# Kernel optimization log

Hardware: AMD Instinct MI355X
Metric: run time of the kernel (lower is better)

Reference implementation:

```python
import jax, jax.numpy as jnp
from jax import lax
import numpy as np

B, N, NPOINT, NSAMPLE = 16, 4096, 1024, 32
RADIUS = 0.2
D_FEAT = 64
IN_CH = 3 + D_FEAT
MLP = (64, 64, 128)
EPS = 1e-5


def fps(xyz, npoint):
    # farthest point sampling, xyz: [B,N,3] -> idx [B,npoint] (start at index 0)
    Bn, Nn, _ = xyz.shape
    batch = jnp.arange(Bn)

    def step(carry, _):
        dist, far = carry                      # dist [B,N], far [B]
        centroid = xyz[batch, far]             # [B,3]
        d = jnp.sum((xyz - centroid[:, None, :]) ** 2, -1)
        dist = jnp.minimum(dist, d)
        new_far = jnp.argmax(dist, -1).astype(jnp.int32)
        return (dist, new_far), far

    init = (jnp.full((Bn, Nn), 1e10, xyz.dtype), jnp.zeros((Bn,), jnp.int32))
    _, idxs = lax.scan(step, init, None, length=npoint)
    return jnp.transpose(idxs)                 # [B, npoint]


def square_distance(a, b):
    # a [B,S,3], b [B,N,3] -> [B,S,N]
    return (jnp.sum(a * a, -1)[:, :, None]
            + jnp.sum(b * b, -1)[:, None, :]
            - 2.0 * jnp.einsum('bsc,bnc->bsn', a, b))


def query_ball(radius, nsample, xyz, new_xyz):
    Nn = xyz.shape[1]
    sqr = square_distance(new_xyz, xyz)                      # [B,S,N]
    gi = jnp.where(sqr > radius ** 2, Nn, jnp.arange(Nn, dtype=jnp.int32))
    gi = jnp.sort(gi, axis=-1)[:, :, :nsample]               # [B,S,K]
    first = gi[:, :, :1]
    return jnp.where(gi == Nn, first, gi)


def gather_points(pts, idx):
    # pts [B,N,C], idx [B,...] -> [B,...,C]
    return jax.vmap(lambda p, i: p[i])(pts, idx)


def _forward(xyz, points, params):
    x = jnp.transpose(xyz, (0, 2, 1))          # [B,N,3]
    p = jnp.transpose(points, (0, 2, 1))       # [B,N,D]
    fidx = fps(x, NPOINT)                      # [B,S]
    new_xyz = gather_points(x, fidx)           # [B,S,3]
    idx = query_ball(RADIUS, NSAMPLE, x, new_xyz)  # [B,S,K]
    g_xyz = gather_points(x, idx)              # [B,S,K,3]
    g_norm = g_xyz - new_xyz[:, :, None, :]
    g_pts = gather_points(p, idx)              # [B,S,K,D]
    feat = jnp.concatenate([g_norm, g_pts], -1)  # [B,S,K,3+D]
    h = jnp.transpose(feat, (0, 3, 2, 1))      # [B,C,K,S]
    for (w, b, g, bt) in params:
        h = jnp.einsum('bcks,oc->boks', h, w) + b[None, :, None, None]
        m = jnp.mean(h, axis=(0, 2, 3), keepdims=True)
        v = jnp.mean((h - m) ** 2, axis=(0, 2, 3), keepdims=True)  # biased var (train BN)
        h = g[None, :, None, None] * (h - m) * lax.rsqrt(v + EPS) + bt[None, :, None, None]
        h = jax.nn.relu(h)
    new_points = jnp.max(h, axis=2)            # [B,Cout,S]
    return jnp.transpose(new_xyz, (0, 2, 1)), new_points


def setup_inputs() -> dict:
    key = jax.random.key(0)
    ks = jax.random.split(key, 16)
    xyz = jax.random.uniform(ks[0], (B, 3, N), dtype=jnp.float32)
    points = jax.random.normal(ks[1], (B, D_FEAT, N), dtype=jnp.float32)
    inp = {'xyz': xyz, 'points': points}
    cin = IN_CH
    for l, cout in enumerate(MLP):
        scale = 1.0 / np.sqrt(cin)
        inp[f'w{l}'] = jax.random.normal(ks[2 + 4 * l], (cout, cin), dtype=jnp.float32) * scale
        inp[f'b{l}'] = jax.random.normal(ks[3 + 4 * l], (cout,), dtype=jnp.float32) * scale
        inp[f'g{l}'] = jnp.ones((cout,), jnp.float32)
        inp[f'bt{l}'] = jnp.zeros((cout,), jnp.float32)
        cin = cout
    return inp


def reference(xyz, points, w0, b0, g0, bt0, w1, b1, g1, bt1, w2, b2, g2, bt2):
    params = [(w0, b0, g0, bt0), (w1, b1, g1, bt1), (w2, b2, g2, bt2)]
    return _forward(xyz, points, params)
```

## Files before the change

kernel.cpp:

```cpp
#include <hip/hip_runtime.h>
#include <stdint.h>

#define NB    16
#define NN    4096
#define NP    1024
#define NS    32
#define NGRP  (NB*NP)
#define CNT   524288.0

typedef short  bf16x8 __attribute__((ext_vector_type(8)));
typedef float  f32x4  __attribute__((ext_vector_type(4)));

__device__ __forceinline__ float bf2f(unsigned short u) {
    return __uint_as_float(((unsigned)u) << 16);
}
__device__ __forceinline__ unsigned short f2bf(float f) {
    unsigned u = __float_as_uint(f);
    unsigned r = u + 0x7fffu + ((u >> 16) & 1u);
    return (unsigned short)(r >> 16);
}
__device__ __forceinline__ bf16x8 as_bf(uint4 u) {
    union { uint4 a; bf16x8 b; } c; c.a = u; return c.b;
}

template <int CTRL, int RM>
__device__ __forceinline__ unsigned long long dppmax(unsigned long long k) {
    int lo = (int)(unsigned)k;
    int hi = (int)(k >> 32);
    int ml = __builtin_amdgcn_update_dpp(lo, lo, CTRL, RM, 0xf, false);
    int mh = __builtin_amdgcn_update_dpp(hi, hi, CTRL, RM, 0xf, false);
    unsigned long long m = ((unsigned long long)(unsigned)mh << 32) | (unsigned)ml;
    return m > k ? m : k;
}

__global__ __launch_bounds__(256, 1) void fps_t_kernel(const float* __restrict__ xyz,
                                                       const float* __restrict__ points,
                                                       const float* __restrict__ w0,
                                                       int* __restrict__ fidx,
                                                       unsigned short* __restrict__ T) {
    if (blockIdx.x >= 16) {
        int gid = (blockIdx.x - 16) * 256 + threadIdx.x;
        int b = gid >> 12, n = gid & (NN - 1);
        const float* xb = xyz + (size_t)b * 3 * NN;
        const float* pb = points + (size_t)b * 64 * NN;
        float acc[64];
#pragma unroll
        for (int o = 0; o < 64; o++) acc[o] = 0.f;
        for (int c = 0; c < 67; c++) {
            float v = (c < 3) ? xb[c * NN + n] : pb[(c - 3) * NN + n];
#pragma unroll
            for (int o = 0; o < 64; o++) acc[o] = fmaf(v, w0[o * 67 + c], acc[o]);
        }
        unsigned short* dst = T + (size_t)gid * 64;
        for (int oo = 0; oo < 64; oo += 8) {
            union { unsigned short u[8]; uint4 v; } r;
#pragma unroll
            for (int j = 0; j < 8; j++) r.u[j] = f2bf(acc[oo + j]);
            *(uint4*)&dst[oo] = r.v;
        }
        return;
    }
    int b = blockIdx.x, tid = threadIdx.x;
    const float* xb = xyz + (size_t)b * 3 * NN;
    __shared__ float4 sxyz4[NN];
    __shared__ unsigned long long red[2][4];
    __shared__ int fbuf[NP];
    float px[16], py[16], pz[16], dist[16];
#pragma unroll
    for (int i = 0; i < 16; i++) {
        int n = i * 256 + tid;
        px[i] = xb[n]; py[i] = xb[NN + n]; pz[i] = xb[2 * NN + n];
        sxyz4[n] = make_float4(px[i], py[i], pz[i], 0.f);
        dist[i] = 1e10f;
    }
#pragma unroll
    for (int i = 0; i < 16; i++) {
        asm volatile("" : "+v"(px[i]));
        asm volatile("" : "+v"(py[i]));
        asm volatile("" : "+v"(pz[i]));
    }
    int wv = tid >> 6;
    if (tid == 0) fbuf[0] = 0;
    int far = 0;
    __syncthreads();
    for (int t = 0; t < NP; t++) {
        float4 c = sxyz4[far];
        float cx = c.x, cy = c.y, cz = c.z;
        float bv = -1.0f; int bi = 0;
#pragma unroll
        for (int i = 0; i < 16; i++) {
            float dx = __fsub_rn(px[i], cx);
            float dy = __fsub_rn(py[i], cy);
            float dz = __fsub_rn(pz[i], cz);
            float d = __fadd_rn(__fadd_rn(__fmul_rn(dx, dx), __fmul_rn(dy, dy)),
                                __fmul_rn(dz, dz));
            float nd = fminf(dist[i], d);
            dist[i] = nd;
            if (nd > bv) { bv = nd; bi = i; }
        }
        int n_best = bi * 256 + tid;
        unsigned long long k =
            ((unsigned long long)__float_as_uint(bv) << 32) |
            (unsigned long long)(~(unsigned)n_best);
        k = dppmax<0x111, 0xf>(k);
        k = dppmax<0x112, 0xf>(k);
        k = dppmax<0x114, 0xf>(k);
        k = dppmax<0x118, 0xf>(k);
        k = dppmax<0x142, 0xa>(k);
        k = dppmax<0x143, 0xc>(k);
        if ((tid & 63) == 63) red[t & 1][wv] = k;
        __syncthreads();
        ulonglong2 ra = *(ulonglong2*)&red[t & 1][0];
        ulonglong2 rb = *(ulonglong2*)&red[t & 1][2];
        unsigned long long r0 = ra.x, r1 = ra.y, r2 = rb.x, r3 = rb.y;
        if (r1 > r0) r0 = r1;
        if (r3 > r2) r2 = r3;
        if (r2 > r0) r0 = r2;
        far = (int)(~(unsigned)r0);
        if (tid == 0 && t + 1 < NP) fbuf[t + 1] = far;
    }
    __syncthreads();
    for (int i = tid; i < NP; i += 256) fidx[b * NP + i] = fbuf[i];
}

__global__ __launch_bounds__(256) void group_kernel(const float* __restrict__ xyz,
                                                    const unsigned short* __restrict__ T,
                                                    const int* __restrict__ fidx,
                                                    int* __restrict__ idx,
                                                    const float* __restrict__ w0,
                                                    const float* __restrict__ b0,
                                                    double* __restrict__ stage1,
                                                    float* __restrict__ out0) {
    __shared__ int gidx[4][NS];
    int t = threadIdx.x, wv = t >> 6, lane = t & 63;
    int g = blockIdx.x * 4 + wv;
    int b = g >> 10, s = g & 1023;
    const float* xb = xyz + (size_t)b * 3 * NN;
    int fid = fidx[g];
    float cx = xb[fid], cy = xb[NN + fid], cz = xb[2 * NN + fid];
    if (lane < 3) {
        float v = (lane == 0) ? cx : ((lane == 1) ? cy : cz);
        out0[((size_t)b * 3 + lane) * NP + s] = v;
    }
    float sa = __fadd_rn(__fadd_rn(__fmul_rn(cx, cx), __fmul_rn(cy, cy)),
                         __fmul_rn(cz, cz));
    int* out = idx + (size_t)g * NS;
    int total = 0; int first = 0;
    for (int ci = 0; ci < NN / 64; ci++) {
        int n = ci * 64 + lane;
        float x = xb[n], y = xb[NN + n], z = xb[2 * NN + n];
        float sb = __fadd_rn(__fadd_rn(__fmul_rn(x, x), __fmul_rn(y, y)),
                             __fmul_rn(z, z));
        float dot = __fadd_rn(__fadd_rn(__fmul_rn(x, cx), __fmul_rn(y, cy)),
                              __fmul_rn(z, cz));
        float sqr = __fsub_rn(__fadd_rn(sa, sb), __fmul_rn(2.0f, dot));
        bool pred = !(sqr > 0.04f);
        unsigned long long mask = __ballot(pred);
        if (mask) {
            if (total == 0) first = ci * 64 + (int)__builtin_ctzll(mask);
            int pos = total + (int)__popcll(mask & ((1ull << lane) - 1ull));
            if (pred && pos < NS) { out[pos] = n; gidx[wv][pos] = n; }
            total += (int)__popcll(mask);
            if (total >= NS) break;
        }
    }
    if (total < NS) {
        if (lane >= total && lane < NS) { out[lane] = first; gidx[wv][lane] = first; }
    }
    int o = lane;
    float uo = fmaf(w0[o * 67 + 2], cz, fmaf(w0[o * 67 + 1], cy, w0[o * 67] * cx));
    float bo = b0[o];
    const unsigned short* Tb = T + (size_t)b * NN * 64;
    float s1 = 0.f, s2 = 0.f;
    for (int k = 0; k < NS; k++) {
        int n = gidx[wv][k];
        float tv = bf2f(Tb[(size_t)n * 64 + o]);
        float h = tv - uo + bo;
        s1 += h; s2 = fmaf(h, h, s2);
    }
    int slot = g & 63;
    atomicAdd(&stage1[slot * 128 + o], (double)s1);
    atomicAdd(&stage1[slot * 128 + 64 + o], (double)s2);
}

__global__ void finalize_kernel(const double* __restrict__ stage, int C,
                                const float* __restrict__ gamma,
                                const float* __restrict__ beta,
                                float* __restrict__ AB) {
    int o = threadIdx.x;
    double s = 0.0, q = 0.0;
    for (int i = 0; i < 64; i++) {
        s += stage[i * 2 * C + o];
        q += stage[i * 2 * C + C + o];
    }
    double m = s * (1.0 / CNT);
    double v = q * (1.0 / CNT) - m * m;
    double A = (double)gamma[o] / sqrt(v + 1e-5);
    AB[o] = (float)A;
    AB[C + o] = (float)((double)beta[o] - m * A);
}

__global__ __launch_bounds__(256) void layer2_kernel(const float* __restrict__ xyz,
                                                     const unsigned short* __restrict__ T,
                                                     const int* __restrict__ fidx,
                                                     const int* __restrict__ idx,
                                                     const float* __restrict__ w0,
                                                     const float* __restrict__ b0,
                                                     const float* __restrict__ AB1,
                                                     const float* __restrict__ w1,
                                                     const float* __restrict__ b1,
                                                     unsigned short* __restrict__ h2,
                                                     double* __restrict__ stage2) {
    __shared__ __attribute__((aligned(16))) unsigned short w1s[64][72];
    __shared__ __attribute__((aligned(16))) unsigned short h1s[4][32][72];
    __shared__ float psum[64], psq[64];
    int t = threadIdx.x, wv = t >> 6, lane = t & 63;
    int quad = lane >> 4, col = lane & 15;
    int g = blockIdx.x * 4 + wv;
    int b = g >> 10;
    for (int lin = t; lin < 4096; lin += 256)
        w1s[lin >> 6][lin & 63] = f2bf(w1[lin]);
    if (t < 64) { psum[t] = 0.f; psq[t] = 0.f; }
    {
        int fid = fidx[g];
        const float* xb = xyz + (size_t)b * 3 * NN;
        float cx = xb[fid], cy = xb[NN + fid], cz = xb[2 * NN + fid];
        int o = lane;
        float uo = fmaf(w0[o * 67 + 2], cz, fmaf(w0[o * 67 + 1], cy, w0[o * 67] * cx));
        float bo = b0[o];
        float a1 = AB1[o], bb1 = AB1[64 + o];
        const int* gi = idx + (size_t)g * NS;
        const unsigned short* Tb = T + (size_t)b * NN * 64;
        for (int k = 0; k < NS; k++) {
            int n = gi[k];
            float tv = bf2f(Tb[(size_t)n * 64 + o]);
            float h = tv - uo + bo;
            float hn = fmaxf(fmaf(h, a1, bb1), 0.f);
            h1s[wv][k][o] = f2bf(hn);
        }
    }
    __syncthreads();
    f32x4 acc[2][4];
#pragma unroll
    for (int i = 0; i < 2; i++)
#pragma unroll
        for (int j = 0; j < 4; j++) acc[i][j] = (f32x4){0.f, 0.f, 0.f, 0.f};
#pragma unroll
    for (int ks = 0; ks < 2; ks++) {
        bf16x8 a0 = as_bf(*(const uint4*)&h1s[wv][col][ks * 32 + quad * 8]);
        bf16x8 a1f = as_bf(*(const uint4*)&h1s[wv][16 + col][ks * 32 + quad * 8]);
#pragma unroll
        for (int nt = 0; nt < 4; nt++) {
            bf16x8 bf = as_bf(*(const uint4*)&w1s[nt * 16 + col][ks * 32 + quad * 8]);
            acc[0][nt] = __builtin_amdgcn_mfma_f32_16x16x32_bf16(a0, bf, acc[0][nt], 0, 0, 0);
            acc[1][nt] = __builtin_amdgcn_mfma_f32_16x16x32_bf16(a1f, bf, acc[1][nt], 0, 0, 0);
        }
    }
    float s1[4], s2[4];
#pragma unroll
    for (int nt = 0; nt < 4; nt++) {
        float bb = b1[nt * 16 + col];
        s1[nt] = 0.f; s2[nt] = 0.f;
#pragma unroll
        for (int mt = 0; mt < 2; mt++)
#pragma unroll
            for (int r = 0; r < 4; r++) {
                float v = acc[mt][nt][r] + bb;
                s1[nt] += v; s2[nt] = fmaf(v, v, s2[nt]);
                h1s[wv][mt * 16 + quad * 4 + r][nt * 16 + col] = f2bf(v);
            }
        s1[nt] += __shfl_xor(s1[nt], 16); s1[nt] += __shfl_xor(s1[nt], 32);
        s2[nt] += __shfl_xor(s2[nt], 16); s2[nt] += __shfl_xor(s2[nt], 32);
        if (quad == 0) {
            atomicAdd(&psum[nt * 16 + col], s1[nt]);
            atomicAdd(&psq[nt * 16 + col], s2[nt]);
        }
    }
#pragma unroll
    for (int r = 0; r < 4; r++) {
        int lin = lane + 64 * r;
        int row = lin >> 3, c = lin & 7;
        uint4 v = *(const uint4*)&h1s[wv][row][c * 8];
        *(uint4*)&h2[((size_t)g * NS + row) * 64 + c * 8] = v;
    }
    __syncthreads();
    if (t < 64) {
        int slot = blockIdx.x & 63;
        atomicAdd(&stage2[slot * 128 + t], (double)psum[t]);
        atomicAdd(&stage2[slot * 128 + 64 + t], (double)psq[t]);
    }
}

__global__ __launch_bounds__(256) void layer3_kernel(const unsigned short* __restrict__ h2,
                                                     const float* __restrict__ AB2,
                                                     const float* __restrict__ w2,
                                                     const float* __restrict__ b2,
                                                     double* __restrict__ stage3,
                                                     float* __restrict__ mxbuf,
                                                     float* __restrict__ mnbuf) {
    __shared__ __attribute__((aligned(16))) unsigned short w2s[128][72];
    __shared__ __attribute__((aligned(16))) unsigned short h2s[4][32][72];
    __shared__ float psum[128], psq[128];
    int t = threadIdx.x, wv = t >> 6, lane = t & 63;
    int quad = lane >> 4, col = lane & 15;
    int g = blockIdx.x * 4 + wv;
    for (int lin = t; lin < 8192; lin += 256)
        w2s[lin >> 6][lin & 63] = f2bf(w2[lin]);
    if (t < 128) { psum[t] = 0.f; psq[t] = 0.f; }
    {
        int c = lane & 7;
        float a2v[8], bb2v[8];
#pragma unroll
        for (int j = 0; j < 8; j++) {
            a2v[j] = AB2[c * 8 + j];
            bb2v[j] = AB2[64 + c * 8 + j];
        }
        const unsigned short* hg = h2 + (size_t)g * NS * 64;
#pragma unroll
        for (int r = 0; r < 4; r++) {
            int row = (lane >> 3) + 8 * r;
            union { uint4 v; unsigned short u[8]; } in, outp;
            in.v = *(const uint4*)&hg[row * 64 + c * 8];
#pragma unroll
            for (int j = 0; j < 8; j++) {
                float f = bf2f(in.u[j]);
                outp.u[j] = f2bf(fmaxf(fmaf(f, a2v[j], bb2v[j]), 0.f));
            }
            *(uint4*)&h2s[wv][row][c * 8] = outp.v;
        }
    }
    __syncthreads();
    f32x4 acc[2][8];
#pragma unroll
    for (int i = 0; i < 2; i++)
#pragma unroll
        for (int j = 0; j < 8; j++) acc[i][j] = (f32x4){0.f, 0.f, 0.f, 0.f};
#pragma unroll
    for (int ks = 0; ks < 2; ks++) {
        bf16x8 a0 = as_bf(*(const uint4*)&h2s[wv][col][ks * 32 + quad * 8]);
        bf16x8 a1f = as_bf(*(const uint4*)&h2s[wv][16 + col][ks * 32 + quad * 8]);
#pragma unroll
        for (int nt = 0; nt < 8; nt++) {
            bf16x8 bf = as_bf(*(const uint4*)&w2s[nt * 16 + col][ks * 32 + quad * 8]);
            acc[0][nt] = __builtin_amdgcn_mfma_f32_16x16x32_bf16(a0, bf, acc[0][nt], 0, 0, 0);
            acc[1][nt] = __builtin_amdgcn_mfma_f32_16x16x32_bf16(a1f, bf, acc[1][nt], 0, 0, 0);
        }
    }
#pragma unroll
    for (int nt = 0; nt < 8; nt++) {
        float bb = b2[nt * 16 + col];
        float s1 = 0.f, s2 = 0.f, mx = -1e30f, mn = 1e30f;
#pragma unroll
        for (int mt = 0; mt < 2; mt++)
#pragma unroll
            for (int r = 0; r < 4; r++) {
                float v = acc[mt][nt][r] + bb;
                s1 += v; s2 = fmaf(v, v, s2);
                mx = fmaxf(mx, v); mn = fminf(mn, v);
            }
        s1 += __shfl_xor(s1, 16); s1 += __shfl_xor(s1, 32);
        s2 += __shfl_xor(s2, 16); s2 += __shfl_xor(s2, 32);
        mx = fmaxf(mx, __shfl_xor(mx, 16)); mx = fmaxf(mx, __shfl_xor(mx, 32));
        mn = fminf(mn, __shfl_xor(mn, 16)); mn = fminf(mn, __shfl_xor(mn, 32));
        if (quad == 0) {
            atomicAdd(&psum[nt * 16 + col], s1);
            atomicAdd(&psq[nt * 16 + col], s2);
            mxbuf[(size_t)g * 128 + nt * 16 + col] = mx;
            mnbuf[(size_t)g * 128 + nt * 16 + col] = mn;
        }
    }
    __syncthreads();
    if (t < 128) {
        int slot = blockIdx.x & 63;
        atomicAdd(&stage3[slot * 256 + t], (double)psum[t]);
        atomicAdd(&stage3[slot * 256 + 128 + t], (double)psq[t]);
    }
}

__global__ __launch_bounds__(256) void epilogue_kernel(const float* __restrict__ mxbuf,
                                                       const float* __restrict__ mnbuf,
                                                       const float* __restrict__ AB3,
                                                       float* __restrict__ out1) {
    __shared__ float tile[32][65];
    int blk = blockIdx.x;
    int b = blk >> 6; int rem = blk & 63;
    int o0 = (rem >> 4) * 32; int s0 = (rem & 15) * 64;
    int t = threadIdx.x;
#pragma unroll
    for (int j = 0; j < 8; j++) {
        int lin = t + 256 * j;
        int sl = lin >> 5, ol = lin & 31;
        int o = o0 + ol;
        float a = AB3[o], bb = AB3[128 + o];
        size_t src = ((size_t)b * NP + s0 + sl) * 128 + o;
        float v = (a >= 0.f) ? mxbuf[src] : mnbuf[src];
        tile[ol][sl] = fmaxf(fmaf(v, a, bb), 0.f);
    }
    __syncthreads();
#pragma unroll
    for (int j = 0; j < 8; j++) {
        int lin = t + 256 * j;
        int ol = lin >> 6, sl = lin & 63;
        out1[((size_t)b * 128 + o0 + ol) * NP + s0 + sl] = tile[ol][sl];
    }
}

extern "C" void kernel_launch(void* const* d_in, const int* in_sizes, int n_in,
                              void* d_out, int out_size, void* d_ws, size_t ws_size,
                              hipStream_t stream) {
    const float* xyz    = (const float*)d_in[0];
    const float* points = (const float*)d_in[1];
    const float* w0  = (const float*)d_in[2];
    const float* b0  = (const float*)d_in[3];
    const float* g0  = (const float*)d_in[4];
    const float* bt0 = (const float*)d_in[5];
    const float* w1  = (const float*)d_in[6];
    const float* b1  = (const float*)d_in[7];
    const float* g1  = (const float*)d_in[8];
    const float* bt1 = (const float*)d_in[9];
    const float* w2  = (const float*)d_in[10];
    const float* b2  = (const float*)d_in[11];
    const float* g2  = (const float*)d_in[12];
    const float* bt2 = (const float*)d_in[13];

    char* ws = (char*)d_ws;
    int*            fidx = (int*)(ws + 0);
    int*            idx  = (int*)(ws + 65536);
    unsigned short* T    = (unsigned short*)(ws + 2162688);
    unsigned short* h2   = (unsigned short*)(ws + 10551296);
    float*          mxbuf = (float*)(ws + 77660160);
    float*          mnbuf = (float*)(ws + 86048768);
    double*         stage = (double*)(ws + 94437376);
    float*          AB   = (float*)(ws + 94699520);
    double* stage1 = stage;
    double* stage2 = stage + 64 * 128;
    double* stage3 = stage + 2 * 64 * 128;
    float* AB1 = AB; float* AB2 = AB + 128; float* AB3 = AB + 256;
    float* out0 = (float*)d_out;
    float* out1 = out0 + NB * 3 * NP;

    hipMemsetAsync(stage, 0, 262144, stream);

    fps_t_kernel<<<16 + 256, 256, 0, stream>>>(xyz, points, w0, fidx, T);
    group_kernel<<<NGRP / 4, 256, 0, stream>>>(xyz, T, fidx, idx, w0, b0, stage1, out0);
    finalize_kernel<<<1, 64, 0, stream>>>(stage1, 64, g0, bt0, AB1);
    layer2_kernel<<<NGRP / 4, 256, 0, stream>>>(xyz, T, fidx, idx, w0, b0, AB1,
                                                w1, b1, h2, stage2);
    finalize_kernel<<<1, 64, 0, stream>>>(stage2, 64, g1, bt1, AB2);
    layer3_kernel<<<NGRP / 4, 256, 0, stream>>>(h2, AB2, w2, b2, stage3, mxbuf, mnbuf);
    finalize_kernel<<<1, 128, 0, stream>>>(stage3, 128, g2, bt2, AB3);
    epilogue_kernel<<<1024, 256, 0, stream>>>(mxbuf, mnbuf, AB3, out1);
}
```

Measured before the change: 836.0 us.

## Fuse FPS, first-layer transform and grouping into one persistent kernel with flag-based streaming

```diff
diff --git a/kernel.cpp b/kernel.cpp
--- a/kernel.cpp
+++ b/kernel.cpp
@@ -7,6 +7,7 @@
 #define NS    32
 #define NGRP  (NB*NP)
 #define CNT   524288.0
+#define NWRK  240
 
 typedef short  bf16x8 __attribute__((ext_vector_type(8)));
 typedef float  f32x4  __attribute__((ext_vector_type(4)));
@@ -33,154 +34,177 @@
     return m > k ? m : k;
 }
 
-__global__ __launch_bounds__(256, 1) void fps_t_kernel(const float* __restrict__ xyz,
+__global__ __launch_bounds__(256, 1) void fused_kernel(const float* __restrict__ xyz,
                                                        const float* __restrict__ points,
                                                        const float* __restrict__ w0,
+                                                       const float* __restrict__ b0,
                                                        int* __restrict__ fidx,
-                                                       unsigned short* __restrict__ T) {
-    if (blockIdx.x >= 16) {
-        int gid = (blockIdx.x - 16) * 256 + threadIdx.x;
-        int b = gid >> 12, n = gid & (NN - 1);
-        const float* xb = xyz + (size_t)b * 3 * NN;
-        const float* pb = points + (size_t)b * 64 * NN;
-        float acc[64];
-#pragma unroll
-        for (int o = 0; o < 64; o++) acc[o] = 0.f;
-        for (int c = 0; c < 67; c++) {
-            float v = (c < 3) ? xb[c * NN + n] : pb[(c - 3) * NN + n];
-#pragma unroll
-            for (int o = 0; o < 64; o++) acc[o] = fmaf(v, w0[o * 67 + c], acc[o]);
-        }
-        unsigned short* dst = T + (size_t)gid * 64;
-        for (int oo = 0; oo < 64; oo += 8) {
-            union { unsigned short u[8]; uint4 v; } r;
-#pragma unroll
-            for (int j = 0; j < 8; j++) r.u[j] = f2bf(acc[oo + j]);
-            *(uint4*)&dst[oo] = r.v;
-        }
-        return;
-    }
-    int b = blockIdx.x, tid = threadIdx.x;
-    const float* xb = xyz + (size_t)b * 3 * NN;
+                                                       unsigned short* __restrict__ T,
+                                                       int* __restrict__ idx,
+                                                       double* __restrict__ stage1,
+                                                       float* __restrict__ out0,
+                                                       int* __restrict__ sync_ctr) {
     __shared__ float4 sxyz4[NN];
     __shared__ unsigned long long red[2][4];
-    __shared__ int fbuf[NP];
-    float px[16], py[16], pz[16], dist[16];
-#pragma unroll
-    for (int i = 0; i < 16; i++) {
-        int n = i * 256 + tid;
-        px[i] = xb[n]; py[i] = xb[NN + n]; pz[i] = xb[2 * NN + n];
-        sxyz4[n] = make_float4(px[i], py[i], pz[i], 0.f);
-        dist[i] = 1e10f;
-    }
-#pragma unroll
-    for (int i = 0; i < 16; i++) {
-        asm volatile("" : "+v"(px[i]));
-        asm volatile("" : "+v"(py[i]));
-        asm volatile("" : "+v"(pz[i]));
-    }
-    int wv = tid >> 6;
-    if (tid == 0) fbuf[0] = 0;
-    int far = 0;
-    __syncthreads();
-    for (int t = 0; t < NP; t++) {
-        float4 c = sxyz4[far];
-        float cx = c.x, cy = c.y, cz = c.z;
-        float bv = -1.0f; int bi = 0;
+    __shared__ int gidx[4][NS];
+    int tid = threadIdx.x;
+    int wv = tid >> 6, lane = tid & 63;
+
+    if (blockIdx.x < 16) {
+        int b = blockIdx.x;
+        const float* xb = xyz + (size_t)b * 3 * NN;
+        float px[16], py[16], pz[16], dist[16];
 #pragma unroll
         for (int i = 0; i < 16; i++) {
-            float dx = __fsub_rn(px[i], cx);
-            float dy = __fsub_rn(py[i], cy);
-            float dz = __fsub_rn(pz[i], cz);
-            float d = __fadd_rn(__fadd_rn(__fmul_rn(dx, dx), __fmul_rn(dy, dy)),
-                                __fmul_rn(dz, dz));
-            float nd = fminf(dist[i], d);
-            dist[i] = nd;
-            if (nd > bv) { bv = nd; bi = i; }
-        }
-        int n_best = bi * 256 + tid;
-        unsigned long long k =
-            ((unsigned long long)__float_as_uint(bv) << 32) |
-            (unsigned long long)(~(unsigned)n_best);
-        k = dppmax<0x111, 0xf>(k);
-        k = dppmax<0x112, 0xf>(k);
-        k = dppmax<0x114, 0xf>(k);
-        k = dppmax<0x118, 0xf>(k);
-        k = dppmax<0x142, 0xa>(k);
-        k = dppmax<0x143, 0xc>(k);
-        if ((tid & 63) == 63) red[t & 1][wv] = k;
+            int n = i * 256 + tid;
+            px[i] = xb[n]; py[i] = xb[NN + n]; pz[i] = xb[2 * NN + n];
+            sxyz4[n] = make_float4(px[i], py[i], pz[i], 0.f);
+            dist[i] = 1e10f;
+        }
+#pragma unroll
+        for (int i = 0; i < 16; i++) {
+            asm volatile("" : "+v"(px[i]));
+            asm volatile("" : "+v"(py[i]));
+            asm volatile("" : "+v"(pz[i]));
+        }
+        int far = 0;
+        if (tid == 0)
+            __hip_atomic_store(&fidx[b * NP], 0, __ATOMIC_RELAXED,
+                               __HIP_MEMORY_SCOPE_AGENT);
         __syncthreads();
-        ulonglong2 ra = *(ulonglong2*)&red[t & 1][0];
-        ulonglong2 rb = *(ulonglong2*)&red[t & 1][2];
-        unsigned long long r0 = ra.x, r1 = ra.y, r2 = rb.x, r3 = rb.y;
-        if (r1 > r0) r0 = r1;
-        if (r3 > r2) r2 = r3;
-        if (r2 > r0) r0 = r2;
-        far = (int)(~(unsigned)r0);
-        if (tid == 0 && t + 1 < NP) fbuf[t + 1] = far;
-    }
-    __syncthreads();
-    for (int i = tid; i < NP; i += 256) fidx[b * NP + i] = fbuf[i];
-}
-
-__global__ __launch_bounds__(256) void group_kernel(const float* __restrict__ xyz,
-                                                    const unsigned short* __restrict__ T,
-                                                    const int* __restrict__ fidx,
-                                                    int* __restrict__ idx,
-                                                    const float* __restrict__ w0,
-                                                    const float* __restrict__ b0,
-                                                    double* __restrict__ stage1,
-                                                    float* __restrict__ out0) {
-    __shared__ int gidx[4][NS];
-    int t = threadIdx.x, wv = t >> 6, lane = t & 63;
-    int g = blockIdx.x * 4 + wv;
-    int b = g >> 10, s = g & 1023;
-    const float* xb = xyz + (size_t)b * 3 * NN;
-    int fid = fidx[g];
-    float cx = xb[fid], cy = xb[NN + fid], cz = xb[2 * NN + fid];
-    if (lane < 3) {
-        float v = (lane == 0) ? cx : ((lane == 1) ? cy : cz);
-        out0[((size_t)b * 3 + lane) * NP + s] = v;
-    }
-    float sa = __fadd_rn(__fadd_rn(__fmul_rn(cx, cx), __fmul_rn(cy, cy)),
-                         __fmul_rn(cz, cz));
-    int* out = idx + (size_t)g * NS;
-    int total = 0; int first = 0;
-    for (int ci = 0; ci < NN / 64; ci++) {
-        int n = ci * 64 + lane;
-        float x = xb[n], y = xb[NN + n], z = xb[2 * NN + n];
-        float sb = __fadd_rn(__fadd_rn(__fmul_rn(x, x), __fmul_rn(y, y)),
-                             __fmul_rn(z, z));
-        float dot = __fadd_rn(__fadd_rn(__fmul_rn(x, cx), __fmul_rn(y, cy)),
-                              __fmul_rn(z, cz));
-        float sqr = __fsub_rn(__fadd_rn(sa, sb), __fmul_rn(2.0f, dot));
-        bool pred = !(sqr > 0.04f);
-        unsigned long long mask = __ballot(pred);
-        if (mask) {
-            if (total == 0) first = ci * 64 + (int)__builtin_ctzll(mask);
-            int pos = total + (int)__popcll(mask & ((1ull << lane) - 1ull));
-            if (pred && pos < NS) { out[pos] = n; gidx[wv][pos] = n; }
-            total += (int)__popcll(mask);
-            if (total >= NS) break;
-        }
-    }
-    if (total < NS) {
-        if (lane >= total && lane < NS) { out[lane] = first; gidx[wv][lane] = first; }
-    }
-    int o = lane;
-    float uo = fmaf(w0[o * 67 + 2], cz, fmaf(w0[o * 67 + 1], cy, w0[o * 67] * cx));
-    float bo = b0[o];
-    const unsigned short* Tb = T + (size_t)b * NN * 64;
-    float s1 = 0.f, s2 = 0.f;
-    for (int k = 0; k < NS; k++) {
-        int n = gidx[wv][k];
-        float tv = bf2f(Tb[(size_t)n * 64 + o]);
-        float h = tv - uo + bo;
-        s1 += h; s2 = fmaf(h, h, s2);
-    }
-    int slot = g & 63;
-    atomicAdd(&stage1[slot * 128 + o], (double)s1);
-    atomicAdd(&stage1[slot * 128 + 64 + o], (double)s2);
+        for (int t = 0; t < NP; t++) {
+            float4 c = sxyz4[far];
+            float cx = c.x, cy = c.y, cz = c.z;
+            float bv = -1.0f; int bi = 0;
+#pragma unroll
+            for (int i = 0; i < 16; i++) {
+                float dx = __fsub_rn(px[i], cx);
+                float dy = __fsub_rn(py[i], cy);
+                float dz = __fsub_rn(pz[i], cz);
+                float d = __fadd_rn(__fadd_rn(__fmul_rn(dx, dx), __fmul_rn(dy, dy)),
+                                    __fmul_rn(dz, dz));
+                float nd = fminf(dist[i], d);
+                dist[i] = nd;
+                if (nd > bv) { bv = nd; bi = i; }
+            }
+            int n_best = bi * 256 + tid;
+            unsigned long long k =
+                ((unsigned long long)__float_as_uint(bv) << 32) |
+                (unsigned long long)(~(unsigned)n_best);
+            k = dppmax<0x111, 0xf>(k);
+            k = dppmax<0x112, 0xf>(k);
+            k = dppmax<0x114, 0xf>(k);
+            k = dppmax<0x118, 0xf>(k);
+            k = dppmax<0x142, 0xa>(k);
+            k = dppmax<0x143, 0xc>(k);
+            if ((tid & 63) == 63) red[t & 1][wv] = k;
+            __syncthreads();
+            ulonglong2 ra = *(ulonglong2*)&red[t & 1][0];
+            ulonglong2 rb = *(ulonglong2*)&red[t & 1][2];
+            unsigned long long r0 = ra.x, r1 = ra.y, r2 = rb.x, r3 = rb.y;
+            if (r1 > r0) r0 = r1;
+            if (r3 > r2) r2 = r3;
+            if (r2 > r0) r0 = r2;
+            far = (int)(~(unsigned)r0);
+            if (tid == 0 && t + 1 < NP)
+                __hip_atomic_store(&fidx[b * NP + t + 1], far, __ATOMIC_RELAXED,
+                                   __HIP_MEMORY_SCOPE_AGENT);
+        }
+        return;
+    }
+
+    int w = blockIdx.x - 16;
+    for (int j = 0; j < 2; j++) {
+        int gid = w * 256 + tid + j * (NWRK * 256);
+        if (gid < NB * NN) {
+            int b = gid >> 12, n = gid & (NN - 1);
+            const float* xb = xyz + (size_t)b * 3 * NN;
+            const float* pb = points + (size_t)b * 64 * NN;
+            float acc[64];
+#pragma unroll
+            for (int o = 0; o < 64; o++) acc[o] = 0.f;
+            for (int c = 0; c < 67; c++) {
+                float v = (c < 3) ? xb[c * NN + n] : pb[(c - 3) * NN + n];
+#pragma unroll
+                for (int o = 0; o < 64; o++) acc[o] = fmaf(v, w0[o * 67 + c], acc[o]);
+            }
+            unsigned short* dst = T + (size_t)gid * 64;
+            for (int oo = 0; oo < 64; oo += 8) {
+                union { unsigned short u[8]; uint4 v; } r;
+#pragma unroll
+                for (int jj = 0; jj < 8; jj++) r.u[jj] = f2bf(acc[oo + jj]);
+                *(uint4*)&dst[oo] = r.v;
+            }
+        }
+    }
+    __syncthreads();
+    __threadfence();
+    if (tid == 0) {
+        __hip_atomic_fetch_add(sync_ctr, 1, __ATOMIC_ACQ_REL, __HIP_MEMORY_SCOPE_AGENT);
+        while (__hip_atomic_load(sync_ctr, __ATOMIC_ACQUIRE, __HIP_MEMORY_SCOPE_AGENT) < NWRK)
+            __builtin_amdgcn_s_sleep(32);
+    }
+    __syncthreads();
+    __threadfence();
+
+    for (int q = w; q < NGRP / 4; q += NWRK) {
+        int g = q * 4 + wv;
+        int b = g >> 10, s = g & 1023;
+        const float* xb = xyz + (size_t)b * 3 * NN;
+        int fid;
+        if (lane == 0) {
+            fid = __hip_atomic_load(&fidx[g], __ATOMIC_RELAXED, __HIP_MEMORY_SCOPE_AGENT);
+            while (fid < 0) {
+                __builtin_amdgcn_s_sleep(16);
+                fid = __hip_atomic_load(&fidx[g], __ATOMIC_RELAXED, __HIP_MEMORY_SCOPE_AGENT);
+            }
+        }
+        fid = __shfl(fid, 0);
+        float cx = xb[fid], cy = xb[NN + fid], cz = xb[2 * NN + fid];
+        if (lane < 3) {
+            float v = (lane == 0) ? cx : ((lane == 1) ? cy : cz);
+            out0[((size_t)b * 3 + lane) * NP + s] = v;
+        }
+        float sa = __fadd_rn(__fadd_rn(__fmul_rn(cx, cx), __fmul_rn(cy, cy)),
+                             __fmul_rn(cz, cz));
+        int* out = idx + (size_t)g * NS;
+        int total = 0; int first = 0;
+        for (int ci = 0; ci < NN / 64; ci++) {
+            int n = ci * 64 + lane;
+            float x = xb[n], y = xb[NN + n], z = xb[2 * NN + n];
+            float sb = __fadd_rn(__fadd_rn(__fmul_rn(x, x), __fmul_rn(y, y)),
+                                 __fmul_rn(z, z));
+            float dot = __fadd_rn(__fadd_rn(__fmul_rn(x, cx), __fmul_rn(y, cy)),
+                                  __fmul_rn(z, cz));
+            float sqr = __fsub_rn(__fadd_rn(sa, sb), __fmul_rn(2.0f, dot));
+            bool pred = !(sqr > 0.04f);
+            unsigned long long mask = __ballot(pred);
+            if (mask) {
+                if (total == 0) first = ci * 64 + (int)__builtin_ctzll(mask);
+                int pos = total + (int)__popcll(mask & ((1ull << lane) - 1ull));
+                if (pred && pos < NS) { out[pos] = n; gidx[wv][pos] = n; }
+                total += (int)__popcll(mask);
+                if (total >= NS) break;
+            }
+        }
+        if (total < NS) {
+            if (lane >= total && lane < NS) { out[lane] = first; gidx[wv][lane] = first; }
+        }
+        int o = lane;
+        float uo = fmaf(w0[o * 67 + 2], cz, fmaf(w0[o * 67 + 1], cy, w0[o * 67] * cx));
+        float bo = b0[o];
+        const unsigned short* Tb = T + (size_t)b * NN * 64;
+        float s1 = 0.f, s2 = 0.f;
+        for (int k = 0; k < NS; k++) {
+            int n = gidx[wv][k];
+            float tv = bf2f(Tb[(size_t)n * 64 + o]);
+            float h = tv - uo + bo;
+            s1 += h; s2 = fmaf(h, h, s2);
+        }
+        int slot = g & 63;
+        atomicAdd(&stage1[slot * 128 + o], (double)s1);
+        atomicAdd(&stage1[slot * 128 + 64 + o], (double)s2);
+    }
 }
 
 __global__ void finalize_kernel(const double* __restrict__ stage, int C,
@@ -432,6 +456,7 @@
     float*          mnbuf = (float*)(ws + 86048768);
     double*         stage = (double*)(ws + 94437376);
     float*          AB   = (float*)(ws + 94699520);
+    int*            sync_ctr = (int*)(ws + 94701312);
     double* stage1 = stage;
     double* stage2 = stage + 64 * 128;
     double* stage3 = stage + 2 * 64 * 128;
@@ -440,9 +465,11 @@
     float* out1 = out0 + NB * 3 * NP;
 
     hipMemsetAsync(stage, 0, 262144, stream);
-
-    fps_t_kernel<<<16 + 256, 256, 0, stream>>>(xyz, points, w0, fidx, T);
-    group_kernel<<<NGRP / 4, 256, 0, stream>>>(xyz, T, fidx, idx, w0, b0, stage1, out0);
+    hipMemsetAsync(fidx, 0xFF, NB * NP * 4, stream);
+    hipMemsetAsync(sync_ctr, 0, 4, stream);
+
+    fused_kernel<<<256, 256, 0, stream>>>(xyz, points, w0, b0, fidx, T, idx,
+                                          stage1, out0, sync_ctr);
     finalize_kernel<<<1, 64, 0, stream>>>(stage1, 64, g0, bt0, AB1);
     layer2_kernel<<<NGRP / 4, 256, 0, stream>>>(xyz, T, fidx, idx, w0, b0, AB1,
                                                 w1, b1, h2, stage2);
```

Measured after the change: 930.0 us. 11.2% more time.
